# Kernel tuning notes

Measured on AMD Instinct MI355X. Metric: run time of the kernel, lower is better.

The kernel has to match this reference:

```python
import jax, jax.numpy as jnp
import numpy as np

DICT_SIZE = 16384
D_MODEL = 1024
TOP_K = 8
B, T = 2, 2048


def setup_inputs() -> dict:
    key = jax.random.key(0)
    k1, k2, k3 = jax.random.split(key, 3)
    x = jax.random.normal(k1, (B, T, D_MODEL), dtype=jnp.float32)
    # nn.Linear weight, scaled small like the torch init style
    W_enc = jax.random.normal(k2, (DICT_SIZE, D_MODEL), dtype=jnp.float32) * 0.02
    # unified dictionary: randn * 0.02 per UnifiedDictionaryCore
    W_dict = jax.random.normal(k3, (DICT_SIZE, D_MODEL), dtype=jnp.float32) * 0.02
    return {"x": x, "W_enc": W_enc, "W_dict": W_dict}


def reference(x, W_enc, W_dict):
    # encoder: Linear(d_model -> dict_size), no bias
    coeffs = jnp.einsum("btd,md->btm", x, W_enc)  # [B,T,dict_size]
    topk_vals, topk_idx = jax.lax.top_k(coeffs, TOP_K)  # [B,T,K]
    # scatter-into-zeros then dense matmul == weighted sum of gathered dict rows
    # (top-k indices are unique per token, so the math is identical)
    rows = W_dict[topk_idx]  # [B,T,K,d_model]
    offset = jnp.einsum("btk,btkd->btd", topk_vals, rows)
    # sparse_coeffs.abs().mean() over the full dense [B,T,dict_size] tensor;
    # only the top-k entries are nonzero
    sparsity_loss = jnp.sum(jnp.abs(topk_vals)) / (coeffs.size)
    return offset, sparsity_loss
```

## Files before the change

### kernel.cpp

```cpp
#include <hip/hip_runtime.h>
#include <float.h>
#include <stdint.h>

constexpr int D_MODEL = 1024;
constexpr int DICT    = 16384;
constexpr int TOPK    = 8;
constexpr int NCAND   = 16;
constexpr int NTOK    = 4096;
constexpr int NTILE   = 128;
constexpr long long COEFF_COUNT = (long long)NTOK * DICT;

typedef __attribute__((ext_vector_type(8))) __bf16 bf16x8;
typedef __attribute__((ext_vector_type(4))) float  floatx4;

__device__ __forceinline__ unsigned short f2bf(float f) {
    unsigned int u = __float_as_uint(f);
    u = u + 0x7fffu + ((u >> 16) & 1u);
    return (unsigned short)(u >> 16);
}

__device__ __forceinline__ void async16(void* lds, const void* g) {
    __builtin_amdgcn_global_load_lds(
        (__attribute__((address_space(1))) void*)g,
        (__attribute__((address_space(3))) void*)lds, 16, 0, 0);
}

__global__ __launch_bounds__(256) void ssod_cvt2(const float4* __restrict__ xs, ushort4* __restrict__ xd, int nx4,
                                                 const float4* __restrict__ ws, ushort4* __restrict__ wd, int nw4) {
    const int i = blockIdx.x * 256 + threadIdx.x;
    if (i < nx4) {
        const float4 v = xs[i];
        ushort4 o; o.x = f2bf(v.x); o.y = f2bf(v.y); o.z = f2bf(v.z); o.w = f2bf(v.w);
        xd[i] = o;
    } else {
        const int j = i - nx4;
        if (j < nw4) {
            const float4 v = ws[j];
            ushort4 o; o.x = f2bf(v.x); o.y = f2bf(v.y); o.z = f2bf(v.z); o.w = f2bf(v.w);
            wd[j] = o;
        }
    }
}

constexpr size_t R1OFF = (size_t)128 * (D_MODEL * 2);

#define STAGE_A(buf_, t_) do {                                               \
    const char* s_ = pA + (size_t)(t_) * 64;                                 \
    char* d_ = (char*)&As[(buf_)][0] + wave * 1024;                          \
    async16(d_, s_); async16(d_ + 8192, s_ + R1OFF);                         \
} while (0)

#define STAGE_B(buf_, t_) do {                                               \
    const char* s_ = pB + (size_t)(t_) * 64;                                 \
    char* d_ = (char*)&Bs[(buf_)][0] + wave * 1024;                          \
    async16(d_, s_); async16(d_ + 8192, s_ + R1OFF);                         \
} while (0)

#define LOADFRAGS(P, buf_) do {                                              \
    const char* ab_ = (const char*)As + (buf_) * 16384 + aob;                \
    const char* bb_ = (const char*)Bs + (buf_) * 16384 + bob;                \
    P##af0 = *(const bf16x8*)(ab_);                                          \
    P##af1 = *(const bf16x8*)(ab_ + 1024);                                   \
    P##af2 = *(const bf16x8*)(ab_ + 2048);                                   \
    P##af3 = *(const bf16x8*)(ab_ + 3072);                                   \
    P##af4 = *(const bf16x8*)(ab_ + 4096);                                   \
    P##af5 = *(const bf16x8*)(ab_ + 5120);                                   \
    P##af6 = *(const bf16x8*)(ab_ + 6144);                                   \
    P##af7 = *(const bf16x8*)(ab_ + 7168);                                   \
    P##bq0 = *(const bf16x8*)(bb_);                                          \
    P##bq1 = *(const bf16x8*)(bb_ + 1024);                                   \
    P##bq2 = *(const bf16x8*)(bb_ + 2048);                                   \
    P##bq3 = *(const bf16x8*)(bb_ + 3072);                                   \
} while (0)

#define MROW(P, AF, m_)                                                                     \
    acc[m_][0] = __builtin_amdgcn_mfma_f32_16x16x32_bf16(P##bq0, AF, acc[m_][0], 0, 0, 0);  \
    acc[m_][1] = __builtin_amdgcn_mfma_f32_16x16x32_bf16(P##bq1, AF, acc[m_][1], 0, 0, 0);  \
    acc[m_][2] = __builtin_amdgcn_mfma_f32_16x16x32_bf16(P##bq2, AF, acc[m_][2], 0, 0, 0);  \
    acc[m_][3] = __builtin_amdgcn_mfma_f32_16x16x32_bf16(P##bq3, AF, acc[m_][3], 0, 0, 0);

#define C1(P) MROW(P, P##af0, 0) MROW(P, P##af1, 1) MROW(P, P##af2, 2) MROW(P, P##af3, 3)
#define C2(P) MROW(P, P##af4, 4) MROW(P, P##af5, 5) MROW(P, P##af6, 6) MROW(P, P##af7, 7)

#define TILE(T_, CONS, LOAD, DOSTAGE, VMI) do {                              \
    if (DOSTAGE) {                                                           \
        STAGE_A(((T_) + 3) & 3, (T_) + 3);                                   \
        STAGE_B(((T_) + 3) & 3, (T_) + 3);                                   \
    }                                                                        \
    asm volatile("s_waitcnt vmcnt(" #VMI ")" ::: "memory");                  \
    asm volatile("s_barrier" ::: "memory");                                  \
    LOADFRAGS(LOAD, ((T_) + 1) & 3);                                         \
    __builtin_amdgcn_s_setprio(1);                                           \
    C1(CONS)                                                                 \
    C2(CONS)                                                                 \
    __builtin_amdgcn_s_setprio(0);                                           \
} while (0)

__global__ __launch_bounds__(512, 2) void ssod_gemm_bf16(const unsigned short* __restrict__ A,
                                                         const unsigned short* __restrict__ B,
                                                         unsigned short* __restrict__ C,
                                                         unsigned short* __restrict__ tmax) {
    __shared__ __align__(16) unsigned short As[4][8192];
    __shared__ __align__(16) unsigned short Bs[4][8192];

    const int tid  = threadIdx.x;
    const int wave = tid >> 6;
    const int lane = tid & 63;

    const int bid = blockIdx.x;
    const int bn  = (bid & 7) * 8 + ((bid >> 3) & 7);
    const int bm  = bid >> 6;

    const int wm = wave >> 2;
    const int wn = wave & 3;
    const int fr = lane & 15;
    const int kg = lane >> 4;

    const int sR   = tid >> 3;
    const int sinp = ((tid & 7) * 16) ^ ((sR & 7) << 4);
    const int smr  = 2 * sR + (sinp >> 6);
    const int skb  = sinp & 63;
    const char* pA = (const char*)(A + (size_t)bm * 256 * D_MODEL) + (size_t)smr * (D_MODEL * 2) + skb;
    const char* pB = (const char*)(B + (size_t)bn * 256 * D_MODEL) + (size_t)smr * (D_MODEL * 2) + skb;

    const int swz = ((((fr & 1) << 6) | (kg << 4)) ^ (((fr >> 1) & 7) << 4));
    const int aob = (wm * 64 + (fr >> 1)) * 128 + swz;
    const int bob = (wn * 32 + (fr >> 1)) * 128 + swz;

    floatx4 acc[8][4];
    #pragma unroll
    for (int i = 0; i < 8; ++i)
        #pragma unroll
        for (int j = 0; j < 4; ++j) acc[i][j] = floatx4{0.f, 0.f, 0.f, 0.f};

    bf16x8 RA_af0, RA_af1, RA_af2, RA_af3, RA_af4, RA_af5, RA_af6, RA_af7;
    bf16x8 RA_bq0, RA_bq1, RA_bq2, RA_bq3;
    bf16x8 RB_af0, RB_af1, RB_af2, RB_af3, RB_af4, RB_af5, RB_af6, RB_af7;
    bf16x8 RB_bq0, RB_bq1, RB_bq2, RB_bq3;

    STAGE_A(0, 0); STAGE_B(0, 0);
    STAGE_A(1, 1); STAGE_B(1, 1);
    STAGE_A(2, 2); STAGE_B(2, 2);
    asm volatile("s_waitcnt vmcnt(8)" ::: "memory");
    asm volatile("s_barrier" ::: "memory");
    LOADFRAGS(RA_, 0);

    #pragma unroll 1
    for (int T = 0; T < 28; T += 2) {
        TILE(T,     RA_, RB_, true, 8);
        TILE(T + 1, RB_, RA_, true, 8);
    }
    TILE(28, RA_, RB_, true,  8);
    TILE(29, RB_, RA_, false, 4);
    TILE(30, RA_, RB_, false, 0);
    __builtin_amdgcn_s_setprio(1);
    C1(RB_)
    C2(RB_)
    __builtin_amdgcn_s_setprio(0);

    __syncthreads();
    unsigned int* rmax = (unsigned int*)&As[0][0];
    rmax[tid] = 0;
    __syncthreads();

    const int tcol  = lane & 15;
    const int rq4   = (lane >> 4) * 4;
    const int half  = wn >> 1;
    const int dbase = bn * 256 + wn * 64 + rq4;

    #pragma unroll
    for (int mf = 0; mf < 8; ++mf) {
        const int tok = wm * 128 + mf * 16 + tcol;
        unsigned int tm = 0;
        #pragma unroll
        for (int nf = 0; nf < 4; ++nf) {
            const floatx4 a = acc[mf][nf];
            const unsigned int b0 = f2bf(a[0]), b1 = f2bf(a[1]);
            const unsigned int b2 = f2bf(a[2]), b3 = f2bf(a[3]);
            tm = max(tm, max(max(b0 ^ 0x8000u, b1 ^ 0x8000u),
                             max(b2 ^ 0x8000u, b3 ^ 0x8000u)));
            uint2 pk; pk.x = b0 | (b1 << 16); pk.y = b2 | (b3 << 16);
            *(uint2*)(C + (size_t)(bm * 256 + tok) * DICT + dbase + nf * 16) = pk;
        }
        tm = max(tm, (unsigned int)__shfl_xor((int)tm, 16, 64));
        tm = max(tm, (unsigned int)__shfl_xor((int)tm, 32, 64));
        if (lane < 16) atomicMax(&rmax[tok * 2 + half], tm);
    }
    __syncthreads();
    tmax[(size_t)(bm * 256 + (tid >> 1)) * NTILE + bn * 2 + (tid & 1)] =
        (unsigned short)rmax[tid];
}

#undef TILE
#undef C1
#undef C2
#undef MROW
#undef LOADFRAGS
#undef STAGE_A
#undef STAGE_B

__device__ __forceinline__ bool tk_better(float v1, int i1, float v2, int i2) {
    return (v1 > v2) || (v1 == v2 && i1 < i2);
}

__global__ __launch_bounds__(256) void ssod_select_refine(const unsigned short* __restrict__ coeffs,
                                                          const unsigned short* __restrict__ tmax,
                                                          const float* __restrict__ x,
                                                          const float* __restrict__ Wenc,
                                                          const float* __restrict__ Wdict,
                                                          float* __restrict__ outp,
                                                          float* __restrict__ tsum,
                                                          int tokBase) {
    const int tl   = blockIdx.x;
    const int t    = tokBase + tl;
    const int tid  = threadIdx.x;
    const int lane = tid & 63;
    const int wave = tid >> 6;

    __shared__ unsigned int keys[128];
    __shared__ int   tlist[64];
    __shared__ int   ncnt, kcnt;
    __shared__ unsigned int sTau;
    __shared__ float xs[D_MODEL];
    __shared__ int   cidx[NCAND];
    __shared__ float cval[NCAND];
    __shared__ float sval[TOPK];
    __shared__ int   sidx[TOPK];

    ((float4*)xs)[tid] = ((const float4*)(x + (size_t)t * D_MODEL))[tid];
    if (tid == 0) { ncnt = 0; kcnt = 0; }
    __syncthreads();

    const unsigned short* tmrow = tmax + (size_t)t * NTILE;
    if (wave == 0) {
        const unsigned int u = ((const unsigned int*)tmrow)[lane];
        unsigned int v0 = u & 0xFFFFu, v1 = u >> 16;
        for (int k = 2; k <= 128; k <<= 1) {
            for (int j = k >> 1; j >= 1; j >>= 1) {
                if (j == 64) {
                    const unsigned int a = max(v0, v1), b = min(v0, v1);
                    v0 = a; v1 = b;
                } else {
                    const unsigned int p0 = __shfl_xor(v0, j, 64);
                    const unsigned int p1 = __shfl_xor(v1, j, 64);
                    const bool tm0 = ((lane & j) == 0) ^ ((( lane      ) & k) != 0);
                    const bool tm1 = ((lane & j) == 0) ^ (((lane + 64) & k) != 0);
                    v0 = tm0 ? max(v0, p0) : min(v0, p0);
                    v1 = tm1 ? max(v1, p1) : min(v1, p1);
                }
            }
        }
        if (lane == 15) sTau = v0;
    }
    __syncthreads();
    const unsigned int tau = sTau;

    if (tid < NTILE) {
        if ((unsigned int)tmrow[tid] >= tau) {
            const int p = atomicAdd(&ncnt, 1);
            if (p < 64) tlist[p] = tid;
        }
    }
    __syncthreads();
    const int nq = min(ncnt, 64);

    const uint4* row4 = (const uint4*)(coeffs + (size_t)tl * DICT);
    for (int j = tid; j < nq * 16; j += 256) {
        const int tile = tlist[j >> 4];
        const int sub  = j & 15;
        const uint4 p = row4[tile * 16 + sub];
        unsigned int w[4] = {p.x ^ 0x80008000u, p.y ^ 0x80008000u,
                             p.z ^ 0x80008000u, p.w ^ 0x80008000u};
        const int base = tile * 128 + sub * 8;
        #pragma unroll
        for (int h = 0; h < 4; ++h) {
            const unsigned int lo = w[h] & 0xFFFFu, hi = w[h] >> 16;
            if (lo >= tau) {
                const int q = atomicAdd(&kcnt, 1);
                if (q < 128) keys[q] = (lo << 16) | (unsigned)(16383 - (base + h * 2));
            }
            if (hi >= tau) {
                const int q = atomicAdd(&kcnt, 1);
                if (q < 128) keys[q] = (hi << 16) | (unsigned)(16383 - (base + h * 2 + 1));
            }
        }
    }
    __syncthreads();
    const int m = min(kcnt, 128);
    for (int i = m + tid; i < 128; i += 256) keys[i] = 0;
    __syncthreads();

    if (wave == 0) {
        unsigned int v0 = keys[lane], v1 = keys[lane + 64];
        for (int k = 2; k <= 128; k <<= 1) {
            for (int j = k >> 1; j >= 1; j >>= 1) {
                if (j == 64) {
                    const unsigned int a = max(v0, v1), b = min(v0, v1);
                    v0 = a; v1 = b;
                } else {
                    const unsigned int p0 = __shfl_xor(v0, j, 64);
                    const unsigned int p1 = __shfl_xor(v1, j, 64);
                    const bool tm0 = ((lane & j) == 0) ^ ((( lane      ) & k) != 0);
                    const bool tm1 = ((lane & j) == 0) ^ (((lane + 64) & k) != 0);
                    v0 = tm0 ? max(v0, p0) : min(v0, p0);
                    v1 = tm1 ? max(v1, p1) : min(v1, p1);
                }
            }
        }
        if (lane < NCAND) cidx[lane] = 16383 - (int)(v0 & 0xFFFFu);
    }
    __syncthreads();

    const float4* xs4 = (const float4*)xs;
    float4 xv[4];
    #pragma unroll
    for (int q = 0; q < 4; ++q) xv[q] = xs4[q * 64 + lane];

    float4 wv[4][4];
    #pragma unroll
    for (int s = 0; s < 4; ++s) {
        const float4* wr4 = (const float4*)(Wenc + (size_t)cidx[s * 4 + wave] * D_MODEL);
        #pragma unroll
        for (int q = 0; q < 4; ++q) wv[s][q] = wr4[q * 64 + lane];
    }
    #pragma unroll
    for (int s = 0; s < 4; ++s) {
        float sum = 0.f;
        #pragma unroll
        for (int q = 0; q < 4; ++q)
            sum += xv[q].x * wv[s][q].x + xv[q].y * wv[s][q].y +
                   xv[q].z * wv[s][q].z + xv[q].w * wv[s][q].w;
        #pragma unroll
        for (int off = 32; off > 0; off >>= 1) sum += __shfl_down(sum, off, 64);
        if (lane == 0) cval[s * 4 + wave] = sum;
    }
    __syncthreads();

    if (tid < NCAND) {
        const float v = cval[tid];
        const int  ix = cidx[tid];
        int rank = 0;
        #pragma unroll
        for (int j = 0; j < NCAND; ++j)
            rank += (j != tid) && tk_better(cval[j], cidx[j], v, ix);
        if (rank < TOPK) { sval[rank] = v; sidx[rank] = ix; }
    }
    __syncthreads();
    if (tid == 0) {
        float s = 0.f;
        #pragma unroll
        for (int k = 0; k < TOPK; ++k) s += fabsf(sval[k]);
        tsum[t] = s;
    }

    const int dd = tid * 4;
    float4 a = make_float4(0.f, 0.f, 0.f, 0.f);
    #pragma unroll
    for (int k = 0; k < TOPK; ++k) {
        const float4 r = *(const float4*)(Wdict + (size_t)sidx[k] * D_MODEL + dd);
        const float s = sval[k];
        a.x += s * r.x; a.y += s * r.y; a.z += s * r.z; a.w += s * r.w;
    }
    *(float4*)(outp + (size_t)t * D_MODEL + dd) = a;
}

__global__ __launch_bounds__(256) void ssod_loss(const float* __restrict__ tsum,
                                                 float* __restrict__ out) {
    float s = 0.f;
    for (int i = threadIdx.x; i < NTOK; i += 256) s += tsum[i];
    #pragma unroll
    for (int off = 32; off > 0; off >>= 1) s += __shfl_down(s, off, 64);
    __shared__ float wsum[4];
    if ((threadIdx.x & 63) == 0) wsum[threadIdx.x >> 6] = s;
    __syncthreads();
    if (threadIdx.x == 0) {
        const float tot = wsum[0] + wsum[1] + wsum[2] + wsum[3];
        out[(size_t)NTOK * D_MODEL] = tot / (float)COEFF_COUNT;
    }
}

extern "C" void kernel_launch(void* const* d_in, const int* in_sizes, int n_in,
                              void* d_out, int out_size, void* d_ws, size_t ws_size,
                              hipStream_t stream) {
    const float* x     = (const float*)d_in[0];
    const float* Wenc  = (const float*)d_in[1];
    const float* Wdict = (const float*)d_in[2];
    float* out = (float*)d_out;

    char* ws = (char*)d_ws;
    size_t off = 0;
    unsigned short* xbf  = (unsigned short*)(ws + off); off += (size_t)NTOK * D_MODEL * 2;
    unsigned short* wbf  = (unsigned short*)(ws + off); off += (size_t)DICT * D_MODEL * 2;
    unsigned short* tmax = (unsigned short*)(ws + off); off += (size_t)NTOK * NTILE * 2;
    float* tsum = (float*)(ws + off);                   off += (size_t)NTOK * 4;
    unsigned short* coeffs = (unsigned short*)(ws + off);

    const size_t remain = (ws_size > off) ? (ws_size - off) : 0;
    int chunk = 512;
    if (remain >= (size_t)4096 * DICT * 2) chunk = 4096;
    else if (remain >= (size_t)2048 * DICT * 2) chunk = 2048;
    else if (remain >= (size_t)1024 * DICT * 2) chunk = 1024;

    const int nx4 = NTOK * D_MODEL / 4;
    const int nw4 = DICT * D_MODEL / 4;
    ssod_cvt2<<<(nx4 + nw4 + 255) / 256, 256, 0, stream>>>(
        (const float4*)x, (ushort4*)xbf, nx4, (const float4*)Wenc, (ushort4*)wbf, nw4);

    for (int tokBase = 0; tokBase < NTOK; tokBase += chunk) {
        const int mtiles = chunk / 256;
        ssod_gemm_bf16<<<mtiles * 64, 512, 0, stream>>>(xbf + (size_t)tokBase * D_MODEL, wbf, coeffs,
                                                        tmax + (size_t)tokBase * NTILE);
        ssod_select_refine<<<chunk, 256, 0, stream>>>(coeffs, tmax, x, Wenc, Wdict, out, tsum, tokBase);
    }
    ssod_loss<<<1, 256, 0, stream>>>(tsum, out);
}
```

Measured before the change: 369.2 us.

## Restructure bf16 GEMM main loop into interleaved half-tile phases with double buffering

```diff
diff --git a/kernel.cpp b/kernel.cpp
--- a/kernel.cpp
+++ b/kernel.cpp
@@ -42,66 +42,61 @@
     }
 }
 
-constexpr size_t R1OFF = (size_t)128 * (D_MODEL * 2);
-
-#define STAGE_A(buf_, t_) do {                                               \
-    const char* s_ = pA + (size_t)(t_) * 64;                                 \
-    char* d_ = (char*)&As[(buf_)][0] + wave * 1024;                          \
-    async16(d_, s_); async16(d_ + 8192, s_ + R1OFF);                         \
+#define SGA(buf_, ks_, T_) do {                                              \
+    char* d_ = AsW + (buf_) * 32768 + (ks_) * 16384;                         \
+    const char* s_ = pA + (T_) * 128 + (ks_) * 64;                           \
+    async16(d_, s_); async16(d_ + 8192, s_ + 262144);                        \
 } while (0)
 
-#define STAGE_B(buf_, t_) do {                                               \
-    const char* s_ = pB + (size_t)(t_) * 64;                                 \
-    char* d_ = (char*)&Bs[(buf_)][0] + wave * 1024;                          \
-    async16(d_, s_); async16(d_ + 8192, s_ + R1OFF);                         \
+#define SGB(buf_, ks_, T_) do {                                              \
+    char* d_ = BsW + (buf_) * 32768 + (ks_) * 16384;                         \
+    const char* s_ = pB + (T_) * 128 + (ks_) * 64;                           \
+    async16(d_, s_); async16(d_ + 8192, s_ + 262144);                        \
 } while (0)
 
-#define LOADFRAGS(P, buf_) do {                                              \
-    const char* ab_ = (const char*)As + (buf_) * 16384 + aob;                \
-    const char* bb_ = (const char*)Bs + (buf_) * 16384 + bob;                \
-    P##af0 = *(const bf16x8*)(ab_);                                          \
-    P##af1 = *(const bf16x8*)(ab_ + 1024);                                   \
-    P##af2 = *(const bf16x8*)(ab_ + 2048);                                   \
-    P##af3 = *(const bf16x8*)(ab_ + 3072);                                   \
-    P##af4 = *(const bf16x8*)(ab_ + 4096);                                   \
-    P##af5 = *(const bf16x8*)(ab_ + 5120);                                   \
-    P##af6 = *(const bf16x8*)(ab_ + 6144);                                   \
-    P##af7 = *(const bf16x8*)(ab_ + 7168);                                   \
-    P##bq0 = *(const bf16x8*)(bb_);                                          \
-    P##bq1 = *(const bf16x8*)(bb_ + 1024);                                   \
-    P##bq2 = *(const bf16x8*)(bb_ + 2048);                                   \
-    P##bq3 = *(const bf16x8*)(bb_ + 3072);                                   \
-} while (0)
-
-#define MROW(P, AF, m_)                                                                     \
-    acc[m_][0] = __builtin_amdgcn_mfma_f32_16x16x32_bf16(P##bq0, AF, acc[m_][0], 0, 0, 0);  \
-    acc[m_][1] = __builtin_amdgcn_mfma_f32_16x16x32_bf16(P##bq1, AF, acc[m_][1], 0, 0, 0);  \
-    acc[m_][2] = __builtin_amdgcn_mfma_f32_16x16x32_bf16(P##bq2, AF, acc[m_][2], 0, 0, 0);  \
-    acc[m_][3] = __builtin_amdgcn_mfma_f32_16x16x32_bf16(P##bq3, AF, acc[m_][3], 0, 0, 0);
-
-#define C1(P) MROW(P, P##af0, 0) MROW(P, P##af1, 1) MROW(P, P##af2, 2) MROW(P, P##af3, 3)
-#define C2(P) MROW(P, P##af4, 4) MROW(P, P##af5, 5) MROW(P, P##af6, 6) MROW(P, P##af7, 7)
-
-#define TILE(T_, CONS, LOAD, DOSTAGE, VMI) do {                              \
-    if (DOSTAGE) {                                                           \
-        STAGE_A(((T_) + 3) & 3, (T_) + 3);                                   \
-        STAGE_B(((T_) + 3) & 3, (T_) + 3);                                   \
+#define SGN ((void)0)
+#define VM6 asm volatile("s_waitcnt vmcnt(6)" ::: "memory")
+#define VM0 asm volatile("s_waitcnt vmcnt(0)" ::: "memory")
+#define VMN ((void)0)
+
+#define MR4(m_, AF_)                                                                        \
+    acc[m_][0] = __builtin_amdgcn_mfma_f32_16x16x32_bf16(bq0, AF_, acc[m_][0], 0, 0, 0);    \
+    acc[m_][1] = __builtin_amdgcn_mfma_f32_16x16x32_bf16(bq1, AF_, acc[m_][1], 0, 0, 0);    \
+    acc[m_][2] = __builtin_amdgcn_mfma_f32_16x16x32_bf16(bq2, AF_, acc[m_][2], 0, 0, 0);    \
+    acc[m_][3] = __builtin_amdgcn_mfma_f32_16x16x32_bf16(bq3, AF_, acc[m_][3], 0, 0, 0);
+
+#define PH(buf_, ks_, qm_, RB_, STG_, VM_) do {                              \
+    const char* ap_ = AsC + (buf_) * 32768 + (ks_) * 16384 + aob + (qm_) * 4096; \
+    bf16x8 af0 = *(const bf16x8*)(ap_);                                      \
+    bf16x8 af1 = *(const bf16x8*)(ap_ + 1024);                               \
+    bf16x8 af2 = *(const bf16x8*)(ap_ + 2048);                               \
+    bf16x8 af3 = *(const bf16x8*)(ap_ + 3072);                               \
+    if (RB_) {                                                               \
+        const char* bp_ = BsC + (buf_) * 32768 + (ks_) * 16384 + bob;        \
+        bq0 = *(const bf16x8*)(bp_);                                         \
+        bq1 = *(const bf16x8*)(bp_ + 1024);                                  \
+        bq2 = *(const bf16x8*)(bp_ + 2048);                                  \
+        bq3 = *(const bf16x8*)(bp_ + 3072);                                  \
     }                                                                        \
-    asm volatile("s_waitcnt vmcnt(" #VMI ")" ::: "memory");                  \
+    STG_;                                                                    \
     asm volatile("s_barrier" ::: "memory");                                  \
-    LOADFRAGS(LOAD, ((T_) + 1) & 3);                                         \
+    asm volatile("s_waitcnt lgkmcnt(0)" ::: "memory");                       \
     __builtin_amdgcn_s_setprio(1);                                           \
-    C1(CONS)                                                                 \
-    C2(CONS)                                                                 \
+    MR4((qm_) * 4 + 0, af0)                                                  \
+    MR4((qm_) * 4 + 1, af1)                                                  \
+    MR4((qm_) * 4 + 2, af2)                                                  \
+    MR4((qm_) * 4 + 3, af3)                                                  \
     __builtin_amdgcn_s_setprio(0);                                           \
+    VM_;                                                                     \
+    asm volatile("s_barrier" ::: "memory");                                  \
 } while (0)
 
 __global__ __launch_bounds__(512, 2) void ssod_gemm_bf16(const unsigned short* __restrict__ A,
                                                          const unsigned short* __restrict__ B,
                                                          unsigned short* __restrict__ C,
                                                          unsigned short* __restrict__ tmax) {
-    __shared__ __align__(16) unsigned short As[4][8192];
-    __shared__ __align__(16) unsigned short Bs[4][8192];
+    __shared__ __align__(16) unsigned short As[2][2][8192];
+    __shared__ __align__(16) unsigned short Bs[2][2][8192];
 
     const int tid  = threadIdx.x;
     const int wave = tid >> 6;
@@ -120,46 +115,54 @@
     const int sinp = ((tid & 7) * 16) ^ ((sR & 7) << 4);
     const int smr  = 2 * sR + (sinp >> 6);
     const int skb  = sinp & 63;
-    const char* pA = (const char*)(A + (size_t)bm * 256 * D_MODEL) + (size_t)smr * (D_MODEL * 2) + skb;
-    const char* pB = (const char*)(B + (size_t)bn * 256 * D_MODEL) + (size_t)smr * (D_MODEL * 2) + skb;
+    const char* pA = (const char*)(A + (size_t)bm * 256 * D_MODEL) + (size_t)smr * 2048 + skb;
+    const char* pB = (const char*)(B + (size_t)bn * 256 * D_MODEL) + (size_t)smr * 2048 + skb;
 
     const int swz = ((((fr & 1) << 6) | (kg << 4)) ^ (((fr >> 1) & 7) << 4));
     const int aob = (wm * 64 + (fr >> 1)) * 128 + swz;
     const int bob = (wn * 32 + (fr >> 1)) * 128 + swz;
 
+    const char* AsC = (const char*)As;
+    const char* BsC = (const char*)Bs;
+    char* AsW = (char*)As + tid * 16;
+    char* BsW = (char*)Bs + tid * 16;
+
     floatx4 acc[8][4];
     #pragma unroll
     for (int i = 0; i < 8; ++i)
         #pragma unroll
         for (int j = 0; j < 4; ++j) acc[i][j] = floatx4{0.f, 0.f, 0.f, 0.f};
 
-    bf16x8 RA_af0, RA_af1, RA_af2, RA_af3, RA_af4, RA_af5, RA_af6, RA_af7;
-    bf16x8 RA_bq0, RA_bq1, RA_bq2, RA_bq3;
-    bf16x8 RB_af0, RB_af1, RB_af2, RB_af3, RB_af4, RB_af5, RB_af6, RB_af7;
-    bf16x8 RB_bq0, RB_bq1, RB_bq2, RB_bq3;
-
-    STAGE_A(0, 0); STAGE_B(0, 0);
-    STAGE_A(1, 1); STAGE_B(1, 1);
-    STAGE_A(2, 2); STAGE_B(2, 2);
-    asm volatile("s_waitcnt vmcnt(8)" ::: "memory");
+    bf16x8 bq0, bq1, bq2, bq3;
+
+    SGB(0, 0, 0); SGA(0, 0, 0); SGB(0, 1, 0); SGA(0, 1, 0);
+    SGB(1, 0, 1); SGA(1, 0, 1); SGB(1, 1, 1);
+    asm volatile("s_waitcnt vmcnt(6)" ::: "memory");
     asm volatile("s_barrier" ::: "memory");
-    LOADFRAGS(RA_, 0);
 
     #pragma unroll 1
-    for (int T = 0; T < 28; T += 2) {
-        TILE(T,     RA_, RB_, true, 8);
-        TILE(T + 1, RB_, RA_, true, 8);
-    }
-    TILE(28, RA_, RB_, true,  8);
-    TILE(29, RB_, RA_, false, 4);
-    TILE(30, RA_, RB_, false, 0);
-    __builtin_amdgcn_s_setprio(1);
-    C1(RB_)
-    C2(RB_)
-    __builtin_amdgcn_s_setprio(0);
-
-    __syncthreads();
-    unsigned int* rmax = (unsigned int*)&As[0][0];
+    for (int i = 0; i < 7; ++i) {
+        const int t1 = 2 * i + 1, t2 = 2 * i + 2, t3 = 2 * i + 3;
+        PH(0, 0, 0, 1, SGA(1, 1, t1), VMN);
+        PH(0, 0, 1, 0, SGB(0, 0, t2), VMN);
+        PH(0, 1, 0, 1, SGA(0, 0, t2), VMN);
+        PH(0, 1, 1, 0, SGB(0, 1, t2), VM6);
+        PH(1, 0, 0, 1, SGA(0, 1, t2), VMN);
+        PH(1, 0, 1, 0, SGB(1, 0, t3), VMN);
+        PH(1, 1, 0, 1, SGA(1, 0, t3), VMN);
+        PH(1, 1, 1, 0, SGB(1, 1, t3), VM6);
+    }
+    PH(0, 0, 0, 1, SGA(1, 1, 15), VMN);
+    PH(0, 0, 1, 0, SGN, VMN);
+    PH(0, 1, 0, 1, SGN, VMN);
+    PH(0, 1, 1, 0, SGN, VM0);
+    PH(1, 0, 0, 1, SGN, VMN);
+    PH(1, 0, 1, 0, SGN, VMN);
+    PH(1, 1, 0, 1, SGN, VMN);
+    PH(1, 1, 1, 0, SGN, VMN);
+
+    __syncthreads();
+    unsigned int* rmax = (unsigned int*)&As[0][0][0];
     rmax[tid] = 0;
     __syncthreads();
 
@@ -191,13 +194,14 @@
         (unsigned short)rmax[tid];
 }
 
-#undef TILE
-#undef C1
-#undef C2
-#undef MROW
-#undef LOADFRAGS
-#undef STAGE_A
-#undef STAGE_B
+#undef PH
+#undef MR4
+#undef SGA
+#undef SGB
+#undef SGN
+#undef VM6
+#undef VM0
+#undef VMN
 
 __device__ __forceinline__ bool tk_better(float v1, int i1, float v2, int i2) {
     return (v1 > v2) || (v1 == v2 && i1 < i2);
```

Measured after the change: 371.1 us. About the same (+0.5%).

## Process one token per wavefront in select-refine to remove block barriers

Applied to the files above, without the earlier changes.

```diff
diff --git a/kernel.cpp b/kernel.cpp
--- a/kernel.cpp
+++ b/kernel.cpp
@@ -203,6 +203,11 @@
     return (v1 > v2) || (v1 == v2 && i1 < i2);
 }
 
+__device__ __forceinline__ int lane_prefix(unsigned long long m) {
+    return __builtin_amdgcn_mbcnt_hi((unsigned)(m >> 32),
+           __builtin_amdgcn_mbcnt_lo((unsigned)m, 0));
+}
+
 __global__ __launch_bounds__(256) void ssod_select_refine(const unsigned short* __restrict__ coeffs,
                                                           const unsigned short* __restrict__ tmax,
                                                           const float* __restrict__ x,
@@ -211,157 +216,162 @@
                                                           float* __restrict__ outp,
                                                           float* __restrict__ tsum,
                                                           int tokBase) {
-    const int tl   = blockIdx.x;
+    const int tid  = threadIdx.x;
+    const int wave = tid >> 6;
+    const int lane = tid & 63;
+    const int tl   = blockIdx.x * 4 + wave;
     const int t    = tokBase + tl;
-    const int tid  = threadIdx.x;
-    const int lane = tid & 63;
-    const int wave = tid >> 6;
-
-    __shared__ unsigned int keys[128];
-    __shared__ int   tlist[64];
-    __shared__ int   ncnt, kcnt;
-    __shared__ unsigned int sTau;
-    __shared__ float xs[D_MODEL];
-    __shared__ int   cidx[NCAND];
-    __shared__ float cval[NCAND];
-    __shared__ float sval[TOPK];
-    __shared__ int   sidx[TOPK];
-
-    ((float4*)xs)[tid] = ((const float4*)(x + (size_t)t * D_MODEL))[tid];
-    if (tid == 0) { ncnt = 0; kcnt = 0; }
-    __syncthreads();
+
+    __shared__ unsigned int keys[4][128];
+    __shared__ int   tlist[4][64];
+    __shared__ int   kcnt[4];
+    __shared__ float cval[4][NCAND];
+    __shared__ int   cidxs[4][NCAND];
+    __shared__ float sval[4][TOPK];
+    __shared__ int   sidx[4][TOPK];
+
+    if (lane == 0) kcnt[wave] = 0;
 
     const unsigned short* tmrow = tmax + (size_t)t * NTILE;
-    if (wave == 0) {
-        const unsigned int u = ((const unsigned int*)tmrow)[lane];
-        unsigned int v0 = u & 0xFFFFu, v1 = u >> 16;
-        for (int k = 2; k <= 128; k <<= 1) {
-            for (int j = k >> 1; j >= 1; j >>= 1) {
-                if (j == 64) {
-                    const unsigned int a = max(v0, v1), b = min(v0, v1);
-                    v0 = a; v1 = b;
-                } else {
-                    const unsigned int p0 = __shfl_xor(v0, j, 64);
-                    const unsigned int p1 = __shfl_xor(v1, j, 64);
-                    const bool tm0 = ((lane & j) == 0) ^ ((( lane      ) & k) != 0);
-                    const bool tm1 = ((lane & j) == 0) ^ (((lane + 64) & k) != 0);
-                    v0 = tm0 ? max(v0, p0) : min(v0, p0);
-                    v1 = tm1 ? max(v1, p1) : min(v1, p1);
+    const unsigned int u = ((const unsigned int*)tmrow)[lane];
+    unsigned int v0 = u & 0xFFFFu, v1 = u >> 16;
+    for (int k = 2; k <= 128; k <<= 1) {
+        for (int j = k >> 1; j >= 1; j >>= 1) {
+            if (j == 64) {
+                const unsigned int a = max(v0, v1), b = min(v0, v1);
+                v0 = a; v1 = b;
+            } else {
+                const unsigned int p0 = __shfl_xor(v0, j, 64);
+                const unsigned int p1 = __shfl_xor(v1, j, 64);
+                const bool tm0 = ((lane & j) == 0) ^ ((( lane      ) & k) != 0);
+                const bool tm1 = ((lane & j) == 0) ^ (((lane + 64) & k) != 0);
+                v0 = tm0 ? max(v0, p0) : min(v0, p0);
+                v1 = tm1 ? max(v1, p1) : min(v1, p1);
+            }
+        }
+    }
+    const unsigned int tau = (unsigned int)__shfl((int)v0, 15, 64);
+
+    {
+        const unsigned int lo = u & 0xFFFFu, hi = u >> 16;
+        const unsigned long long b0 = __ballot(lo >= tau);
+        const unsigned long long b1 = __ballot(hi >= tau);
+        const int base1 = __popcll(b0);
+        if (lo >= tau) { const int p = lane_prefix(b0);         if (p < 64) tlist[wave][p] = 2 * lane; }
+        if (hi >= tau) { const int p = base1 + lane_prefix(b1); if (p < 64) tlist[wave][p] = 2 * lane + 1; }
+        const int nqf = min(base1 + __popcll(b1), 64);
+
+        const uint4* row4 = (const uint4*)(coeffs + (size_t)tl * DICT);
+        for (int j = lane; j < nqf * 16; j += 64) {
+            const int tile = tlist[wave][j >> 4];
+            const int sub  = j & 15;
+            const uint4 p = row4[tile * 16 + sub];
+            unsigned int w[4] = {p.x ^ 0x80008000u, p.y ^ 0x80008000u,
+                                 p.z ^ 0x80008000u, p.w ^ 0x80008000u};
+            const int base = tile * 128 + sub * 8;
+            #pragma unroll
+            for (int h = 0; h < 4; ++h) {
+                const unsigned int lo2 = w[h] & 0xFFFFu, hi2 = w[h] >> 16;
+                if (lo2 >= tau) {
+                    const int q = atomicAdd(&kcnt[wave], 1);
+                    if (q < 128) keys[wave][q] = (lo2 << 16) | (unsigned)(16383 - (base + h * 2));
+                }
+                if (hi2 >= tau) {
+                    const int q = atomicAdd(&kcnt[wave], 1);
+                    if (q < 128) keys[wave][q] = (hi2 << 16) | (unsigned)(16383 - (base + h * 2 + 1));
                 }
             }
         }
-        if (lane == 15) sTau = v0;
-    }
-    __syncthreads();
-    const unsigned int tau = sTau;
-
-    if (tid < NTILE) {
-        if ((unsigned int)tmrow[tid] >= tau) {
-            const int p = atomicAdd(&ncnt, 1);
-            if (p < 64) tlist[p] = tid;
-        }
-    }
-    __syncthreads();
-    const int nq = min(ncnt, 64);
-
-    const uint4* row4 = (const uint4*)(coeffs + (size_t)tl * DICT);
-    for (int j = tid; j < nq * 16; j += 256) {
-        const int tile = tlist[j >> 4];
-        const int sub  = j & 15;
-        const uint4 p = row4[tile * 16 + sub];
-        unsigned int w[4] = {p.x ^ 0x80008000u, p.y ^ 0x80008000u,
-                             p.z ^ 0x80008000u, p.w ^ 0x80008000u};
-        const int base = tile * 128 + sub * 8;
-        #pragma unroll
-        for (int h = 0; h < 4; ++h) {
-            const unsigned int lo = w[h] & 0xFFFFu, hi = w[h] >> 16;
-            if (lo >= tau) {
-                const int q = atomicAdd(&kcnt, 1);
-                if (q < 128) keys[q] = (lo << 16) | (unsigned)(16383 - (base + h * 2));
+    }
+    {
+        const int m = min(kcnt[wave], 128);
+        for (int i = m + lane; i < 128; i += 64) keys[wave][i] = 0;
+    }
+
+    v0 = keys[wave][lane]; v1 = keys[wave][lane + 64];
+    for (int k = 2; k <= 128; k <<= 1) {
+        for (int j = k >> 1; j >= 1; j >>= 1) {
+            if (j == 64) {
+                const unsigned int a = max(v0, v1), b = min(v0, v1);
+                v0 = a; v1 = b;
+            } else {
+                const unsigned int p0 = __shfl_xor(v0, j, 64);
+                const unsigned int p1 = __shfl_xor(v1, j, 64);
+                const bool tm0 = ((lane & j) == 0) ^ ((( lane      ) & k) != 0);
+                const bool tm1 = ((lane & j) == 0) ^ (((lane + 64) & k) != 0);
+                v0 = tm0 ? max(v0, p0) : min(v0, p0);
+                v1 = tm1 ? max(v1, p1) : min(v1, p1);
             }
-            if (hi >= tau) {
-                const int q = atomicAdd(&kcnt, 1);
-                if (q < 128) keys[q] = (hi << 16) | (unsigned)(16383 - (base + h * 2 + 1));
-            }
-        }
-    }
-    __syncthreads();
-    const int m = min(kcnt, 128);
-    for (int i = m + tid; i < 128; i += 256) keys[i] = 0;
-    __syncthreads();
-
-    if (wave == 0) {
-        unsigned int v0 = keys[lane], v1 = keys[lane + 64];
-        for (int k = 2; k <= 128; k <<= 1) {
-            for (int j = k >> 1; j >= 1; j >>= 1) {
-                if (j == 64) {
-                    const unsigned int a = max(v0, v1), b = min(v0, v1);
-                    v0 = a; v1 = b;
-                } else {
-                    const unsigned int p0 = __shfl_xor(v0, j, 64);
-                    const unsigned int p1 = __shfl_xor(v1, j, 64);
-                    const bool tm0 = ((lane & j) == 0) ^ ((( lane      ) & k) != 0);
-                    const bool tm1 = ((lane & j) == 0) ^ (((lane + 64) & k) != 0);
-                    v0 = tm0 ? max(v0, p0) : min(v0, p0);
-                    v1 = tm1 ? max(v1, p1) : min(v1, p1);
-                }
-            }
-        }
-        if (lane < NCAND) cidx[lane] = 16383 - (int)(v0 & 0xFFFFu);
-    }
-    __syncthreads();
-
-    const float4* xs4 = (const float4*)xs;
-    float4 xv[4];
+        }
+    }
+    const int my_cidx = 16383 - (int)(v0 & 0xFFFFu);
+    if (lane < NCAND) cidxs[wave][lane] = my_cidx;
+
+    const float4* xr = (const float4*)(x + (size_t)t * D_MODEL);
+    const float4 xv0 = xr[lane], xv1 = xr[lane + 64], xv2 = xr[lane + 128], xv3 = xr[lane + 192];
+
     #pragma unroll
-    for (int q = 0; q < 4; ++q) xv[q] = xs4[q * 64 + lane];
-
-    float4 wv[4][4];
-    #pragma unroll
-    for (int s = 0; s < 4; ++s) {
-        const float4* wr4 = (const float4*)(Wenc + (size_t)cidx[s * 4 + wave] * D_MODEL);
-        #pragma unroll
-        for (int q = 0; q < 4; ++q) wv[s][q] = wr4[q * 64 + lane];
-    }
-    #pragma unroll
-    for (int s = 0; s < 4; ++s) {
-        float sum = 0.f;
-        #pragma unroll
-        for (int q = 0; q < 4; ++q)
-            sum += xv[q].x * wv[s][q].x + xv[q].y * wv[s][q].y +
-                   xv[q].z * wv[s][q].z + xv[q].w * wv[s][q].w;
-        #pragma unroll
-        for (int off = 32; off > 0; off >>= 1) sum += __shfl_down(sum, off, 64);
-        if (lane == 0) cval[s * 4 + wave] = sum;
-    }
-    __syncthreads();
-
-    if (tid < NCAND) {
-        const float v = cval[tid];
-        const int  ix = cidx[tid];
+    for (int p = 0; p < 4; ++p) {
+        const int c0 = __shfl(my_cidx, 4 * p + 0, 64);
+        const int c1 = __shfl(my_cidx, 4 * p + 1, 64);
+        const int c2 = __shfl(my_cidx, 4 * p + 2, 64);
+        const int c3 = __shfl(my_cidx, 4 * p + 3, 64);
+        const float4* w0 = (const float4*)(Wenc + (size_t)c0 * D_MODEL);
+        const float4* w1 = (const float4*)(Wenc + (size_t)c1 * D_MODEL);
+        const float4* w2 = (const float4*)(Wenc + (size_t)c2 * D_MODEL);
+        const float4* w3 = (const float4*)(Wenc + (size_t)c3 * D_MODEL);
+        float s0 = 0.f, s1 = 0.f, s2 = 0.f, s3 = 0.f;
+        #pragma unroll
+        for (int j = 0; j < 4; ++j) {
+            const float4 xj = (j == 0) ? xv0 : (j == 1) ? xv1 : (j == 2) ? xv2 : xv3;
+            const int ix = lane + 64 * j;
+            const float4 a0 = w0[ix]; s0 += a0.x * xj.x + a0.y * xj.y + a0.z * xj.z + a0.w * xj.w;
+            const float4 a1 = w1[ix]; s1 += a1.x * xj.x + a1.y * xj.y + a1.z * xj.z + a1.w * xj.w;
+            const float4 a2 = w2[ix]; s2 += a2.x * xj.x + a2.y * xj.y + a2.z * xj.z + a2.w * xj.w;
+            const float4 a3 = w3[ix]; s3 += a3.x * xj.x + a3.y * xj.y + a3.z * xj.z + a3.w * xj.w;
+        }
+        #pragma unroll
+        for (int off = 32; off > 0; off >>= 1) {
+            s0 += __shfl_down(s0, off, 64);
+            s1 += __shfl_down(s1, off, 64);
+            s2 += __shfl_down(s2, off, 64);
+            s3 += __shfl_down(s3, off, 64);
+        }
+        if (lane == 0) {
+            cval[wave][4 * p + 0] = s0; cval[wave][4 * p + 1] = s1;
+            cval[wave][4 * p + 2] = s2; cval[wave][4 * p + 3] = s3;
+        }
+    }
+
+    if (lane < NCAND) {
+        const float v = cval[wave][lane];
+        const int  ix = cidxs[wave][lane];
         int rank = 0;
         #pragma unroll
         for (int j = 0; j < NCAND; ++j)
-            rank += (j != tid) && tk_better(cval[j], cidx[j], v, ix);
-        if (rank < TOPK) { sval[rank] = v; sidx[rank] = ix; }
-    }
-    __syncthreads();
-    if (tid == 0) {
+            rank += (j != lane) && tk_better(cval[wave][j], cidxs[wave][j], v, ix);
+        if (rank < TOPK) { sval[wave][rank] = v; sidx[wave][rank] = ix; }
+    }
+    if (lane == 0) {
         float s = 0.f;
         #pragma unroll
-        for (int k = 0; k < TOPK; ++k) s += fabsf(sval[k]);
+        for (int k = 0; k < TOPK; ++k) s += fabsf(sval[wave][k]);
         tsum[t] = s;
     }
 
-    const int dd = tid * 4;
-    float4 a = make_float4(0.f, 0.f, 0.f, 0.f);
+    float4 a0 = make_float4(0.f, 0.f, 0.f, 0.f), a1 = a0, a2 = a0, a3 = a0;
     #pragma unroll
     for (int k = 0; k < TOPK; ++k) {
-        const float4 r = *(const float4*)(Wdict + (size_t)sidx[k] * D_MODEL + dd);
-        const float s = sval[k];
-        a.x += s * r.x; a.y += s * r.y; a.z += s * r.z; a.w += s * r.w;
-    }
-    *(float4*)(outp + (size_t)t * D_MODEL + dd) = a;
+        const float s = sval[wave][k];
+        const float4* r = (const float4*)(Wdict + (size_t)sidx[wave][k] * D_MODEL);
+        const float4 r0 = r[lane], r1 = r[lane + 64], r2 = r[lane + 128], r3 = r[lane + 192];
+        a0.x += s * r0.x; a0.y += s * r0.y; a0.z += s * r0.z; a0.w += s * r0.w;
+        a1.x += s * r1.x; a1.y += s * r1.y; a1.z += s * r1.z; a1.w += s * r1.w;
+        a2.x += s * r2.x; a2.y += s * r2.y; a2.z += s * r2.z; a2.w += s * r2.w;
+        a3.x += s * r3.x; a3.y += s * r3.y; a3.z += s * r3.z; a3.w += s * r3.w;
+    }
+    float4* op = (float4*)(outp + (size_t)t * D_MODEL);
+    op[lane] = a0; op[lane + 64] = a1; op[lane + 128] = a2; op[lane + 192] = a3;
 }
 
 __global__ __launch_bounds__(256) void ssod_loss(const float* __restrict__ tsum,
@@ -410,7 +420,7 @@
         const int mtiles = chunk / 256;
         ssod_gemm_bf16<<<mtiles * 64, 512, 0, stream>>>(xbf + (size_t)tokBase * D_MODEL, wbf, coeffs,
                                                         tmax + (size_t)tokBase * NTILE);
-        ssod_select_refine<<<chunk, 256, 0, stream>>>(coeffs, tmax, x, Wenc, Wdict, out, tsum, tokBase);
+        ssod_select_refine<<<chunk / 4, 256, 0, stream>>>(coeffs, tmax, x, Wenc, Wdict, out, tsum, tokBase);
     }
     ssod_loss<<<1, 256, 0, stream>>>(tsum, out);
 }
```

After: 370.5 us. Within noise of the previous version (+0.4%).
